# Kernel optimization log

Hardware: AMD Instinct MI355X
Metric: run time of the kernel (lower is better)

Reference implementation:

```python
import jax, jax.numpy as jnp
import numpy as np

TRUE_CLASS_NUM = 10000   # leaf classes
CLASS_NUM = 16384        # total tree nodes (leaves + internal)
HIDDEN = 512
BATCH = 4096
MAX_DEPTH = 6


def setup_inputs() -> dict:
    key = jax.random.key(0)
    kx, kw, ky = jax.random.split(key, 3)
    x = jax.random.normal(kx, (BATCH, HIDDEN), dtype=jnp.float32)
    y = jax.random.randint(ky, (BATCH,), 0, TRUE_CLASS_NUM, dtype=jnp.int64)
    # linear.weight of nn.Linear(hidden, class_num, bias=False): [class_num, hidden]
    weights = jax.random.normal(kw, (CLASS_NUM, HIDDEN), dtype=jnp.float32) * 0.02
    # new2index: each leaf class j has a path; torch code sums weights[j] plus
    # weights[path[0..len-2]]. We materialize exactly the summed ancestor indices
    # as flat CSR-style (ancestor_idx, segment_id) with variable depth per class.
    rng = np.random.default_rng(0)
    depth = rng.integers(1, MAX_DEPTH + 1, size=TRUE_CLASS_NUM)          # ancestors per class
    ancestor_idx = rng.integers(TRUE_CLASS_NUM, CLASS_NUM, size=int(depth.sum()))
    segment_id = np.repeat(np.arange(TRUE_CLASS_NUM), depth)
    return {
        "x": x,
        "y": y,
        "weights": weights,
        "ancestor_idx": jnp.asarray(ancestor_idx, dtype=jnp.int32),
        "segment_id": jnp.asarray(segment_id, dtype=jnp.int32),
    }


def reference(x, y, weights, ancestor_idx, segment_id):
    # added_weights[j] = weights[j] + sum over ancestors on j's tree path
    anc_sum = jax.ops.segment_sum(weights[ancestor_idx], segment_id,
                                  num_segments=TRUE_CLASS_NUM)  # [T, H]
    added_weights = weights[:TRUE_CLASS_NUM] + anc_sum           # [T, H]
    logits = jnp.einsum('bh,th->bt', x, added_weights)           # [B, T]
    logp = jax.nn.log_softmax(logits, axis=-1)
    loss = -jnp.take_along_axis(logp, y[:, None], axis=1).mean()  # CrossEntropyLoss (mean)
    return (loss, logits)
```

## Files before the change

### kernel.cpp

```cpp
#include <hip/hip_runtime.h>
#include <hip/hip_bf16.h>


typedef __bf16 bf16x8 __attribute__((ext_vector_type(8)));
typedef float f32x4 __attribute__((ext_vector_type(4)));
typedef unsigned short u16x8 __attribute__((ext_vector_type(8)));

#define BATCH 4096
#define HID 512
#define TCLS 10000
#define NPAD 10112

__device__ __forceinline__ unsigned short f2bf(float f) {
    unsigned u = __float_as_uint(f);
    unsigned r = (u + 0x7fffu + ((u >> 16) & 1u)) >> 16;
    return (unsigned short)r;
}

__global__ __launch_bounds__(256) void cvt_x_kernel(const float* __restrict__ x,
                                                    unsigned short* __restrict__ xb, int n) {
    int i = (blockIdx.x * 256 + threadIdx.x) * 4;
    if (i < n) {
        float4 v = *(const float4*)(x + i);
        ushort4 o;
        o.x = f2bf(v.x); o.y = f2bf(v.y); o.z = f2bf(v.z); o.w = f2bf(v.w);
        *(ushort4*)(xb + i) = o;
    }
}

__global__ __launch_bounds__(256) void build_aw_kernel(const float* __restrict__ W,
                                                       const int* __restrict__ anc,
                                                       const int* __restrict__ seg,
                                                       int nnz,
                                                       unsigned short* __restrict__ awb) {
    int j = blockIdx.x;
    int h = threadIdx.x * 2;
    unsigned short* dst = awb + (size_t)j * HID + h;
    if (j >= TCLS) {
        *(ushort2*)dst = make_ushort2(0, 0);
        return;
    }
    int lo = 0, hi = nnz;
    while (lo < hi) { int mid = (lo + hi) >> 1; if (seg[mid] < j) lo = mid + 1; else hi = mid; }
    int start = lo;
    hi = nnz;
    while (lo < hi) { int mid = (lo + hi) >> 1; if (seg[mid] <= j) lo = mid + 1; else hi = mid; }
    int end = lo;
    float2 a = *(const float2*)(W + (size_t)j * HID + h);
    for (int k = start; k < end; k++) {
        float2 w = *(const float2*)(W + (size_t)anc[k] * HID + h);
        a.x += w.x; a.y += w.y;
    }
    ushort2 o; o.x = f2bf(a.x); o.y = f2bf(a.y);
    *(ushort2*)dst = o;
}

#define BM 128
#define BN 128
#define BK 32
__global__ __launch_bounds__(256) void gemm_bt_kernel(const unsigned short* __restrict__ A,
                                                      const unsigned short* __restrict__ B,
                                                      float* __restrict__ C) {
    __shared__ __align__(16) unsigned short lds_a[BM * BK];
    __shared__ __align__(16) unsigned short lds_b[BN * BK];

    const int tid = threadIdx.x;
    const int bm = blockIdx.y * BM;
    const int bn = blockIdx.x * BN;
    const int wave = tid >> 6;
    const int lane = tid & 63;
    const int l15 = lane & 15;
    const int quad = lane >> 4;
    const int wm = (wave >> 1) * 64;
    const int wn = (wave & 1) * 64;

    f32x4 acc[4][4];
#pragma unroll
    for (int i = 0; i < 4; i++)
#pragma unroll
        for (int j = 0; j < 4; j++) acc[i][j] = (f32x4)0.f;

    const int c0 = tid, c1 = tid + 256;
    const unsigned short* a_g0 = A + (size_t)(bm + (c0 >> 2)) * HID + (c0 & 3) * 8;
    const unsigned short* a_g1 = A + (size_t)(bm + (c1 >> 2)) * HID + (c1 & 3) * 8;
    const unsigned short* b_g0 = B + (size_t)(bn + (c0 >> 2)) * HID + (c0 & 3) * 8;
    const unsigned short* b_g1 = B + (size_t)(bn + (c1 >> 2)) * HID + (c1 & 3) * 8;
    unsigned short* a_l0 = &lds_a[c0 * 8];
    unsigned short* a_l1 = &lds_a[c1 * 8];
    unsigned short* b_l0 = &lds_b[c0 * 8];
    unsigned short* b_l1 = &lds_b[c1 * 8];

    for (int k0 = 0; k0 < HID; k0 += BK) {
        u16x8 ra0 = *(const u16x8*)(a_g0 + k0);
        u16x8 ra1 = *(const u16x8*)(a_g1 + k0);
        u16x8 rb0 = *(const u16x8*)(b_g0 + k0);
        u16x8 rb1 = *(const u16x8*)(b_g1 + k0);
        *(u16x8*)a_l0 = ra0;
        *(u16x8*)a_l1 = ra1;
        *(u16x8*)b_l0 = rb0;
        *(u16x8*)b_l1 = rb1;
        __syncthreads();

        bf16x8 af[4], bfr[4];
#pragma unroll
        for (int mt = 0; mt < 4; mt++)
            af[mt] = *(const bf16x8*)&lds_a[(wm + mt * 16 + l15) * BK + quad * 8];
#pragma unroll
        for (int nt = 0; nt < 4; nt++)
            bfr[nt] = *(const bf16x8*)&lds_b[(wn + nt * 16 + l15) * BK + quad * 8];
#pragma unroll
        for (int mt = 0; mt < 4; mt++)
#pragma unroll
            for (int nt = 0; nt < 4; nt++)
                acc[mt][nt] = __builtin_amdgcn_mfma_f32_16x16x32_bf16(af[mt], bfr[nt],
                                                                      acc[mt][nt], 0, 0, 0);
        __syncthreads();
    }

#pragma unroll
    for (int nt = 0; nt < 4; nt++) {
        int col = bn + wn + nt * 16 + l15;
        if (col < TCLS) {
#pragma unroll
            for (int mt = 0; mt < 4; mt++) {
                int row = bm + wm + mt * 16 + quad * 4;
#pragma unroll
                for (int r = 0; r < 4; r++)
                    C[(size_t)(row + r) * TCLS + col] = acc[mt][nt][r];
            }
        }
    }
}

__global__ __launch_bounds__(256) void softmax_loss_kernel(const float* __restrict__ logits,
                                                           const int* __restrict__ y,
                                                           float* __restrict__ terms) {
    int row = blockIdx.x;
    const float* rp = logits + (size_t)row * TCLS;
    float m = -INFINITY, s = 0.f;
    for (int c = threadIdx.x; c < TCLS; c += 256) {
        float v = rp[c];
        float nm = fmaxf(m, v);
        s = s * __expf(m - nm) + __expf(v - nm);
        m = nm;
    }
#pragma unroll
    for (int off = 32; off > 0; off >>= 1) {
        float om = __shfl_down(m, off, 64);
        float os = __shfl_down(s, off, 64);
        float nm = fmaxf(m, om);
        s = s * __expf(m - nm) + os * __expf(om - nm);
        m = nm;
    }
    __shared__ float sm[4], ss[4];
    int w = threadIdx.x >> 6;
    if ((threadIdx.x & 63) == 0) { sm[w] = m; ss[w] = s; }
    __syncthreads();
    if (threadIdx.x == 0) {
        m = sm[0]; s = ss[0];
        for (int i = 1; i < 4; i++) {
            float nm = fmaxf(m, sm[i]);
            s = s * __expf(m - nm) + ss[i] * __expf(sm[i] - nm);
            m = nm;
        }
        terms[row] = m + __logf(s) - rp[y[row]];
    }
}

__global__ __launch_bounds__(256) void reduce_loss_kernel(const float* __restrict__ terms,
                                                          float* __restrict__ out) {
    float s = 0.f;
    for (int i = threadIdx.x; i < BATCH; i += 256) s += terms[i];
#pragma unroll
    for (int off = 32; off > 0; off >>= 1) s += __shfl_down(s, off, 64);
    __shared__ float sh[4];
    if ((threadIdx.x & 63) == 0) sh[threadIdx.x >> 6] = s;
    __syncthreads();
    if (threadIdx.x == 0) out[0] = (sh[0] + sh[1] + sh[2] + sh[3]) * (1.0f / BATCH);
}

extern "C" void kernel_launch(void* const* d_in, const int* in_sizes, int n_in,
                              void* d_out, int out_size, void* d_ws, size_t ws_size,
                              hipStream_t stream) {
    const float* x = (const float*)d_in[0];
    const int* y = (const int*)d_in[1];
    const float* W = (const float*)d_in[2];
    const int* anc = (const int*)d_in[3];
    const int* seg = (const int*)d_in[4];
    int nnz = in_sizes[3];

    unsigned short* xb = (unsigned short*)d_ws;
    unsigned short* awb = xb + (size_t)BATCH * HID;
    float* terms = (float*)(awb + (size_t)NPAD * HID);
    float* loss = (float*)d_out;
    float* logits = loss + 1;

    cvt_x_kernel<<<(BATCH * HID) / (256 * 4), 256, 0, stream>>>(x, xb, BATCH * HID);
    build_aw_kernel<<<NPAD, 256, 0, stream>>>(W, anc, seg, nnz, awb);
    dim3 grid(NPAD / BN, BATCH / BM);
    gemm_bt_kernel<<<grid, 256, 0, stream>>>(xb, awb, logits);
    softmax_loss_kernel<<<BATCH, 256, 0, stream>>>(logits, y, terms);
    reduce_loss_kernel<<<1, 256, 0, stream>>>(terms, loss);
}
```

Baseline: 340.3 us.

## Fuse per-tile softmax partials into GEMM epilogue and stage coalesced logit stores

The GEMM epilogue now computes a per-row max and sum-exp for each 128-column tile and writes these partials to a workspace. A small kernel then merges the 79 partials per row, so the full 164 MB logits array is no longer re-read. Output stores are staged through LDS so global writes are row-contiguous and coalesced. The global loads for the next K step are issued before the MFMA work as a register prefetch. The cost is extra LDS traffic and syncs in the epilogue.

```diff
diff --git a/kernel.cpp b/kernel.cpp
--- a/kernel.cpp
+++ b/kernel.cpp
@@ -10,6 +10,7 @@
 #define HID 512
 #define TCLS 10000
 #define NPAD 10112
+#define NBLK 79
 
 __device__ __forceinline__ unsigned short f2bf(float f) {
     unsigned u = __float_as_uint(f);
@@ -58,11 +59,15 @@
 #define BM 128
 #define BN 128
 #define BK 32
-__global__ __launch_bounds__(256) void gemm_bt_kernel(const unsigned short* __restrict__ A,
-                                                      const unsigned short* __restrict__ B,
-                                                      float* __restrict__ C) {
-    __shared__ __align__(16) unsigned short lds_a[BM * BK];
-    __shared__ __align__(16) unsigned short lds_b[BN * BK];
+__global__ __launch_bounds__(256) void gemm_fused_kernel(const unsigned short* __restrict__ A,
+                                                         const unsigned short* __restrict__ B,
+                                                         float* __restrict__ C,
+                                                         float2* __restrict__ partials) {
+    __shared__ __align__(16) unsigned char smem[32 * 132 * 4];
+    unsigned short* lds_a = (unsigned short*)smem;
+    unsigned short* lds_b = ((unsigned short*)smem) + BM * BK;
+    float* ldsc = (float*)smem;
+    float2* pm = (float2*)smem;
 
     const int tid = threadIdx.x;
     const int bm = blockIdx.y * BM;
@@ -90,17 +95,26 @@
     unsigned short* b_l0 = &lds_b[c0 * 8];
     unsigned short* b_l1 = &lds_b[c1 * 8];
 
+    u16x8 ra0 = *(const u16x8*)a_g0;
+    u16x8 ra1 = *(const u16x8*)a_g1;
+    u16x8 rb0 = *(const u16x8*)b_g0;
+    u16x8 rb1 = *(const u16x8*)b_g1;
+
     for (int k0 = 0; k0 < HID; k0 += BK) {
-        u16x8 ra0 = *(const u16x8*)(a_g0 + k0);
-        u16x8 ra1 = *(const u16x8*)(a_g1 + k0);
-        u16x8 rb0 = *(const u16x8*)(b_g0 + k0);
-        u16x8 rb1 = *(const u16x8*)(b_g1 + k0);
         *(u16x8*)a_l0 = ra0;
         *(u16x8*)a_l1 = ra1;
         *(u16x8*)b_l0 = rb0;
         *(u16x8*)b_l1 = rb1;
         __syncthreads();
 
+        int kn = k0 + BK;
+        if (kn < HID) {
+            ra0 = *(const u16x8*)(a_g0 + kn);
+            ra1 = *(const u16x8*)(a_g1 + kn);
+            rb0 = *(const u16x8*)(b_g0 + kn);
+            rb1 = *(const u16x8*)(b_g1 + kn);
+        }
+
         bf16x8 af[4], bfr[4];
 #pragma unroll
         for (int mt = 0; mt < 4; mt++)
@@ -117,54 +131,96 @@
         __syncthreads();
     }
 
-#pragma unroll
-    for (int nt = 0; nt < 4; nt++) {
-        int col = bn + wn + nt * 16 + l15;
-        if (col < TCLS) {
-#pragma unroll
-            for (int mt = 0; mt < 4; mt++) {
-                int row = bm + wm + mt * 16 + quad * 4;
-#pragma unroll
-                for (int r = 0; r < 4; r++)
-                    C[(size_t)(row + r) * TCLS + col] = acc[mt][nt][r];
+    const int colbase = bn + wn + l15;
+#pragma unroll
+    for (int mt = 0; mt < 4; mt++) {
+#pragma unroll
+        for (int r = 0; r < 4; r++) {
+            float v[4];
+#pragma unroll
+            for (int nt = 0; nt < 4; nt++)
+                v[nt] = (colbase + nt * 16 < TCLS) ? acc[mt][nt][r] : -1e30f;
+            float m = fmaxf(fmaxf(v[0], v[1]), fmaxf(v[2], v[3]));
+#pragma unroll
+            for (int off = 1; off < 16; off <<= 1)
+                m = fmaxf(m, __shfl_xor(m, off, 64));
+            float s = __expf(v[0] - m) + __expf(v[1] - m) +
+                      __expf(v[2] - m) + __expf(v[3] - m);
+#pragma unroll
+            for (int off = 1; off < 16; off <<= 1)
+                s += __shfl_xor(s, off, 64);
+            if (l15 == 0) {
+                int rowl = wm + mt * 16 + quad * 4 + r;
+                pm[rowl * 2 + (wave & 1)] = make_float2(m, s);
             }
         }
     }
-}
-
-__global__ __launch_bounds__(256) void softmax_loss_kernel(const float* __restrict__ logits,
-                                                           const int* __restrict__ y,
-                                                           float* __restrict__ terms) {
-    int row = blockIdx.x;
-    const float* rp = logits + (size_t)row * TCLS;
-    float m = -INFINITY, s = 0.f;
-    for (int c = threadIdx.x; c < TCLS; c += 256) {
-        float v = rp[c];
-        float nm = fmaxf(m, v);
-        s = s * __expf(m - nm) + __expf(v - nm);
+    __syncthreads();
+    if (tid < 128) {
+        float2 p0 = pm[tid * 2 + 0];
+        float2 p1 = pm[tid * 2 + 1];
+        float nm = fmaxf(p0.x, p1.x);
+        float s = p0.y * __expf(p0.x - nm) + p1.y * __expf(p1.x - nm);
+        partials[(size_t)(bm + tid) * NBLK + blockIdx.x] = make_float2(nm, s);
+    }
+    __syncthreads();
+
+#pragma unroll
+    for (int t = 0; t < 4; t++) {
+        if ((wave >> 1) == (t >> 1)) {
+            int mtbase = (t & 1) * 2;
+#pragma unroll
+            for (int mi = 0; mi < 2; mi++) {
+                int mt = mtbase + mi;
+                int rowl = mi * 16 + quad * 4;
+#pragma unroll
+                for (int nt = 0; nt < 4; nt++)
+#pragma unroll
+                    for (int r = 0; r < 4; r++)
+                        ldsc[(rowl + r) * 132 + wn + nt * 16 + l15] = acc[mt][nt][r];
+            }
+        }
+        __syncthreads();
+#pragma unroll
+        for (int e = 0; e < 16; e++) {
+            int idx = e * 256 + tid;
+            int rowl = idx >> 7;
+            int col = idx & 127;
+            int gc = bn + col;
+            if (gc < TCLS)
+                C[(size_t)(bm + t * 32 + rowl) * TCLS + gc] = ldsc[rowl * 132 + col];
+        }
+        __syncthreads();
+    }
+}
+
+__global__ __launch_bounds__(256) void lse_kernel(const float2* __restrict__ partials,
+                                                  const float* __restrict__ logits,
+                                                  const int* __restrict__ y,
+                                                  float* __restrict__ terms) {
+    int row = blockIdx.x * 4 + (threadIdx.x >> 6);
+    int lane = threadIdx.x & 63;
+    float m = -1e30f, s = 0.f;
+    if (lane < NBLK) {
+        float2 p = partials[(size_t)row * NBLK + lane];
+        m = p.x; s = p.y;
+    }
+    if (lane + 64 < NBLK) {
+        float2 p = partials[(size_t)row * NBLK + lane + 64];
+        float nm = fmaxf(m, p.x);
+        s = s * __expf(m - nm) + p.y * __expf(p.x - nm);
         m = nm;
     }
 #pragma unroll
-    for (int off = 32; off > 0; off >>= 1) {
-        float om = __shfl_down(m, off, 64);
-        float os = __shfl_down(s, off, 64);
+    for (int off = 1; off < 64; off <<= 1) {
+        float om = __shfl_xor(m, off, 64);
+        float os = __shfl_xor(s, off, 64);
         float nm = fmaxf(m, om);
         s = s * __expf(m - nm) + os * __expf(om - nm);
         m = nm;
     }
-    __shared__ float sm[4], ss[4];
-    int w = threadIdx.x >> 6;
-    if ((threadIdx.x & 63) == 0) { sm[w] = m; ss[w] = s; }
-    __syncthreads();
-    if (threadIdx.x == 0) {
-        m = sm[0]; s = ss[0];
-        for (int i = 1; i < 4; i++) {
-            float nm = fmaxf(m, sm[i]);
-            s = s * __expf(m - nm) + ss[i] * __expf(sm[i] - nm);
-            m = nm;
-        }
-        terms[row] = m + __logf(s) - rp[y[row]];
-    }
+    if (lane == 0)
+        terms[row] = m + __logf(s) - logits[(size_t)row * TCLS + y[row]];
 }
 
 __global__ __launch_bounds__(256) void reduce_loss_kernel(const float* __restrict__ terms,
@@ -191,14 +247,15 @@
 
     unsigned short* xb = (unsigned short*)d_ws;
     unsigned short* awb = xb + (size_t)BATCH * HID;
-    float* terms = (float*)(awb + (size_t)NPAD * HID);
+    float2* partials = (float2*)(awb + (size_t)NPAD * HID);
+    float* terms = (float*)(partials + (size_t)BATCH * NBLK);
     float* loss = (float*)d_out;
     float* logits = loss + 1;
 
     cvt_x_kernel<<<(BATCH * HID) / (256 * 4), 256, 0, stream>>>(x, xb, BATCH * HID);
     build_aw_kernel<<<NPAD, 256, 0, stream>>>(W, anc, seg, nnz, awb);
     dim3 grid(NPAD / BN, BATCH / BM);
-    gemm_bt_kernel<<<grid, 256, 0, stream>>>(xb, awb, logits);
-    softmax_loss_kernel<<<BATCH, 256, 0, stream>>>(logits, y, terms);
+    gemm_fused_kernel<<<grid, 256, 0, stream>>>(xb, awb, logits, partials);
+    lse_kernel<<<BATCH / 4, 256, 0, stream>>>(partials, logits, y, terms);
     reduce_loss_kernel<<<1, 256, 0, stream>>>(terms, loss);
 }
```

Result: no change. 335.7 us (-1.3%).
